# Performance work log

Measured on AMD Instinct MI355X. Metric: run time of the kernel, lower is better.

Reference implementation:

```python
import itertools
import jax, jax.numpy as jnp
import numpy as np

LATENT_DIM = 8
N = 2 * LATENT_DIM  # width of z_combined = concat([z, dz])
BATCH = 131072

# Static combinatorial index sets, matching the nested-loop order
# (i <= j [<= k]) of the torch implementation exactly.
_PAIRS = np.array(list(itertools.combinations_with_replacement(range(N), 2)), dtype=np.int32)   # [136, 2]
_TRIPLES = np.array(list(itertools.combinations_with_replacement(range(N), 3)), dtype=np.int32)  # [816, 3]


def setup_inputs() -> dict:
    key = jax.random.key(0)
    k1, k2 = jax.random.split(key)
    z = jax.random.normal(k1, (BATCH, LATENT_DIM), dtype=jnp.float32)
    dz = jax.random.normal(k2, (BATCH, LATENT_DIM), dtype=jnp.float32)
    return {"z": z, "dz": dz}


def reference(z, dz):
    # z, dz: [B, latent_dim] -> Theta: [B, 985]
    zc = jnp.concatenate([z, dz], axis=1)  # [B, N]
    B = zc.shape[0]
    ones = jnp.ones((B, 1), dtype=zc.dtype)
    # degree-2 terms: zc[:, i] * zc[:, j] for i <= j, all at once via gather
    deg2 = zc[:, _PAIRS[:, 0]] * zc[:, _PAIRS[:, 1]]  # [B, 136]
    # degree-3 terms: zc[:, i] * zc[:, j] * zc[:, k] for i <= j <= k
    deg3 = zc[:, _TRIPLES[:, 0]] * zc[:, _TRIPLES[:, 1]] * zc[:, _TRIPLES[:, 2]]  # [B, 816]
    sine = jnp.sin(zc)  # [B, N]
    return jnp.concatenate([ones, zc, deg2, deg3, sine], axis=1)  # [B, 985]
```

## Files before the change

kernel.cpp:

```cpp
#include <hip/hip_runtime.h>
#include <cstddef>

#define NCOLS 985
#define TROWS 4
#define TILEF (TROWS * NCOLS)
#define NT4   (TILEF / 4)
#define GSTR  176

__global__ __launch_bounds__(256) void sindy_kernel(const float* __restrict__ z,
                                                    const float* __restrict__ dz,
                                                    float* __restrict__ out, int batch,
                                                    int ntiles) {
  __shared__ unsigned short mtab[1024];
  __shared__ unsigned short ptab[136];
  __shared__ float G[4][GSTR];
  __shared__ alignas(16) float rowbuf[TILEF];

  const int tid = threadIdx.x;

  for (int e = tid; e < 1024; e += 256) {
    int a, b;
    if (e < 153)       { a = (e == 0) ? 0 : e; b = 0; }
    else if (e < 969)  {
      int t = e - 153, i = 0;
      for (;;) { int c = (16 - i) * (17 - i) / 2; if (t < c) break; t -= c; ++i; }
      int j = i; while (t >= 16 - j) { t -= 16 - j; ++j; }
      int k = j + t;
      int p = i * 16 - i * (i - 1) / 2 + (j - i);
      a = 17 + p; b = 1 + k;
    }
    else if (e < 985)  { a = 153 + (e - 969); b = 0; }
    else               { a = 169; b = 169; }
    mtab[e] = (unsigned short)(a | (b << 8));
  }
  for (int e = tid; e < 136; e += 256) {
    int p = e, i = 0; while (p >= 16 - i) { p -= 16 - i; ++i; }
    ptab[e] = (unsigned short)(i | ((i + p) << 4));
  }
  __syncthreads();

  const int w = tid >> 6, l = tid & 63;

  unsigned short mt[16];
  #pragma unroll
  for (int wd = 0; wd < 16; ++wd) mt[wd] = mtab[wd * 64 + l];
  const unsigned pe0 = ptab[l];
  const unsigned pe1 = ptab[64 + l];
  const unsigned pe2 = ptab[(128 + l < 136) ? (128 + l) : 135];

  float* Gw = G[w];

  for (int tile = blockIdx.x; tile < ntiles; tile += gridDim.x) {
    const int trow0 = tile * TROWS;
    const int row   = trow0 + w;
    const int nrows = (batch - trow0 < TROWS) ? (batch - trow0) : TROWS;

    if (row < batch) {
      float gval = 0.f;
      if (l == 0)       gval = 1.0f;
      else if (l < 9)   gval = z [(size_t)row * 8 + (l - 1)];
      else if (l < 17)  gval = dz[(size_t)row * 8 + (l - 9)];
      const int gaddr = (l < 17) ? l : (152 + l);
      if (l < 24) Gw[gaddr] = gval;

      const float sv = __shfl(gval, l + 1);
      if (l < 16) Gw[153 + l] = __sinf(sv);
      __builtin_amdgcn_sched_barrier(0);

      {
        float a0 = Gw[1 + (pe0 & 15)], b0 = Gw[1 + (pe0 >> 4)];
        Gw[17 + l] = a0 * b0;
        float a1 = Gw[1 + (pe1 & 15)], b1 = Gw[1 + (pe1 >> 4)];
        Gw[17 + 64 + l] = a1 * b1;
        if (l < 8) {
          float a2 = Gw[1 + (pe2 & 15)], b2 = Gw[1 + (pe2 >> 4)];
          Gw[17 + 128 + l] = a2 * b2;
        }
      }
      __builtin_amdgcn_sched_barrier(0);

      float* rb = rowbuf + w * NCOLS;
      #pragma unroll
      for (int wd = 0; wd < 16; ++wd) {
        const unsigned e = mt[wd];
        const float v = Gw[e & 255] * Gw[e >> 8];
        if (wd < 15)              rb[wd * 64 + l] = v;
        else if (l < NCOLS - 960) rb[960 + l] = v;
      }
    }
    __syncthreads();

    if (nrows == TROWS) {
      float4* __restrict__ dst = (float4*)(out + (size_t)tile * TILEF);
      const float4* srcq = (const float4*)rowbuf;
      #pragma unroll 4
      for (int u = tid; u < NT4; u += 256) {
        dst[u] = srcq[u];
      }
    } else {
      const int nel = nrows * NCOLS;
      float* __restrict__ dst = out + (size_t)tile * TILEF;
      for (int u = tid; u < nel; u += 256) dst[u] = rowbuf[u];
    }
    __syncthreads();
  }
}

extern "C" void kernel_launch(void* const* d_in, const int* in_sizes, int n_in,
                              void* d_out, int out_size, void* d_ws, size_t ws_size,
                              hipStream_t stream) {
  const float* z  = (const float*)d_in[0];
  const float* dz = (const float*)d_in[1];
  float* out = (float*)d_out;
  const int batch = in_sizes[0] / 8;

  const int ntiles = (batch + TROWS - 1) / TROWS;
  const int blocks = 1792;
  sindy_kernel<<<blocks, 256, 0, stream>>>(z, dz, out, batch, ntiles);
}
```

Baseline: 120.9 us.

## Double-buffer row tiles so compute of the next tile overlaps global stores

Adds a second shared-memory tile buffer so each block stores the previous tile to global memory while computing the next one. This drops one __syncthreads per tile. It also rewrites the cubic-term lookup table to use 16-bit offsets into G, and raises the grid from 1792 to 2048 blocks. Shared memory per block roughly doubles, which may lower occupancy. The store-bound kernel may gain little from the overlap.

Result: faster. 117.2 us (-3.1%).

```diff
diff --git a/kernel.cpp b/kernel.cpp
--- a/kernel.cpp
+++ b/kernel.cpp
@@ -4,34 +4,32 @@
 #define NCOLS 985
 #define TROWS 4
 #define TILEF (TROWS * NCOLS)
-#define NT4   (TILEF / 4)
+#define NU    (TILEF / 4)
 #define GSTR  176
 
 __global__ __launch_bounds__(256) void sindy_kernel(const float* __restrict__ z,
                                                     const float* __restrict__ dz,
                                                     float* __restrict__ out, int batch,
                                                     int ntiles) {
-  __shared__ unsigned short mtab[1024];
+  __shared__ unsigned int ctab[1024];
   __shared__ unsigned short ptab[136];
-  __shared__ float G[4][GSTR];
-  __shared__ alignas(16) float rowbuf[TILEF];
+  __shared__ float G4[4][GSTR];
+  __shared__ alignas(16) float buf[2][TILEF];
 
   const int tid = threadIdx.x;
 
-  for (int e = tid; e < 1024; e += 256) {
-    int a, b;
-    if (e < 153)       { a = (e == 0) ? 0 : e; b = 0; }
-    else if (e < 969)  {
-      int t = e - 153, i = 0;
-      for (;;) { int c = (16 - i) * (17 - i) / 2; if (t < c) break; t -= c; ++i; }
-      int j = i; while (t >= 16 - j) { t -= 16 - j; ++j; }
-      int k = j + t;
-      int p = i * 16 - i * (i - 1) / 2 + (j - i);
-      a = 17 + p; b = 1 + k;
+  for (int c = tid; c < 1024; c += 256) {
+    unsigned goff, midx;
+    if (c < 153)      { goff = (unsigned)c; midx = 0; }
+    else if (c < 969) {
+      int t = c - 153, i = 0;
+      for (;;) { int cnt = (16 - i) * (17 - i) / 2; if (t < cnt) break; t -= cnt; ++i; }
+      goff = (unsigned)(17 + (136 - (16 - i) * (17 - i) / 2) + t);
+      midx = (unsigned)(1 + i);
     }
-    else if (e < 985)  { a = 153 + (e - 969); b = 0; }
-    else               { a = 169; b = 169; }
-    mtab[e] = (unsigned short)(a | (b << 8));
+    else if (c < 985) { goff = (unsigned)(153 + (c - 969)); midx = 0; }
+    else              { goff = 169; midx = 169; }
+    ctab[c] = goff | (midx << 16);
   }
   for (int e = tid; e < 136; e += 256) {
     int p = e, i = 0; while (p >= 16 - i) { p -= 16 - i; ++i; }
@@ -41,68 +39,84 @@
 
   const int w = tid >> 6, l = tid & 63;
 
-  unsigned short mt[16];
+  unsigned ct[16];
   #pragma unroll
-  for (int wd = 0; wd < 16; ++wd) mt[wd] = mtab[wd * 64 + l];
+  for (int s = 0; s < 16; ++s) ct[s] = ctab[s * 64 + l];
   const unsigned pe0 = ptab[l];
   const unsigned pe1 = ptab[64 + l];
   const unsigned pe2 = ptab[(128 + l < 136) ? (128 + l) : 135];
 
-  float* Gw = G[w];
+  float* Gw = G4[w];
 
-  for (int tile = blockIdx.x; tile < ntiles; tile += gridDim.x) {
-    const int trow0 = tile * TROWS;
-    const int row   = trow0 + w;
-    const int nrows = (batch - trow0 < TROWS) ? (batch - trow0) : TROWS;
+  auto compute_row = [&](int row, float* rb) {
+    float gval = 0.f;
+    if (l == 0)       gval = 1.0f;
+    else if (l < 9)   gval = z [(size_t)row * 8 + (l - 1)];
+    else if (l < 17)  gval = dz[(size_t)row * 8 + (l - 9)];
+    const int gaddr = (l < 17) ? l : (152 + l);
+    if (l < 24) Gw[gaddr] = gval;
 
-    if (row < batch) {
-      float gval = 0.f;
-      if (l == 0)       gval = 1.0f;
-      else if (l < 9)   gval = z [(size_t)row * 8 + (l - 1)];
-      else if (l < 17)  gval = dz[(size_t)row * 8 + (l - 9)];
-      const int gaddr = (l < 17) ? l : (152 + l);
-      if (l < 24) Gw[gaddr] = gval;
+    const float sv = __shfl(gval, l + 1);
+    if (l < 16) Gw[153 + l] = __sinf(sv);
+    __builtin_amdgcn_sched_barrier(0);
 
-      const float sv = __shfl(gval, l + 1);
-      if (l < 16) Gw[153 + l] = __sinf(sv);
-      __builtin_amdgcn_sched_barrier(0);
-
-      {
-        float a0 = Gw[1 + (pe0 & 15)], b0 = Gw[1 + (pe0 >> 4)];
-        Gw[17 + l] = a0 * b0;
-        float a1 = Gw[1 + (pe1 & 15)], b1 = Gw[1 + (pe1 >> 4)];
-        Gw[17 + 64 + l] = a1 * b1;
-        if (l < 8) {
-          float a2 = Gw[1 + (pe2 & 15)], b2 = Gw[1 + (pe2 >> 4)];
-          Gw[17 + 128 + l] = a2 * b2;
-        }
-      }
-      __builtin_amdgcn_sched_barrier(0);
-
-      float* rb = rowbuf + w * NCOLS;
-      #pragma unroll
-      for (int wd = 0; wd < 16; ++wd) {
-        const unsigned e = mt[wd];
-        const float v = Gw[e & 255] * Gw[e >> 8];
-        if (wd < 15)              rb[wd * 64 + l] = v;
-        else if (l < NCOLS - 960) rb[960 + l] = v;
+    {
+      float a0 = Gw[1 + (pe0 & 15)], b0 = Gw[1 + (pe0 >> 4)];
+      Gw[17 + l] = a0 * b0;
+      float a1 = Gw[1 + (pe1 & 15)], b1 = Gw[1 + (pe1 >> 4)];
+      Gw[17 + 64 + l] = a1 * b1;
+      if (l < 8) {
+        float a2 = Gw[1 + (pe2 & 15)], b2 = Gw[1 + (pe2 >> 4)];
+        Gw[17 + 128 + l] = a2 * b2;
       }
     }
-    __syncthreads();
+    __builtin_amdgcn_sched_barrier(0);
 
-    if (nrows == TROWS) {
-      float4* __restrict__ dst = (float4*)(out + (size_t)tile * TILEF);
-      const float4* srcq = (const float4*)rowbuf;
-      #pragma unroll 4
-      for (int u = tid; u < NT4; u += 256) {
-        dst[u] = srcq[u];
+    #pragma unroll
+    for (int s = 0; s < 16; ++s) {
+      const unsigned e = ct[s];
+      const float v = Gw[e & 0xffffu] * Gw[e >> 16];
+      if (s < 15)      rb[s * 64 + l] = v;
+      else if (l < 25) rb[960 + l] = v;
+    }
+  };
+
+  auto drain_tile = [&](const float* src, float4* __restrict__ dst, int nelem) {
+    if (nelem == TILEF) {
+      const float4* s4 = (const float4*)src;
+      #pragma unroll
+      for (int k = 0; k < 4; ++k) {
+        const int u = k * 256 + tid;
+        if (k < 3 || u < NU) dst[u] = s4[u];
       }
     } else {
-      const int nel = nrows * NCOLS;
-      float* __restrict__ dst = out + (size_t)tile * TILEF;
-      for (int u = tid; u < nel; u += 256) dst[u] = rowbuf[u];
+      float* __restrict__ d = (float*)dst;
+      for (int u = tid; u < nelem; u += 256) d[u] = src[u];
+    }
+  };
+
+  int t = blockIdx.x;
+  if (t >= ntiles) return;
+  int p = 0;
+  {
+    const int row = t * TROWS + w;
+    if (row < batch) compute_row(row, buf[0] + w * NCOLS);
+  }
+  __syncthreads();
+
+  for (int tn = t + gridDim.x; tn < ntiles; tn += gridDim.x) {
+    const int nel = min(TILEF, batch * NCOLS - t * TILEF);
+    drain_tile(buf[p], (float4*)(out + (size_t)t * TILEF), nel);
+    {
+      const int row = tn * TROWS + w;
+      if (row < batch) compute_row(row, buf[p ^ 1] + w * NCOLS);
     }
     __syncthreads();
+    p ^= 1; t = tn;
+  }
+  {
+    const int nel = min(TILEF, batch * NCOLS - t * TILEF);
+    drain_tile(buf[p], (float4*)(out + (size_t)t * TILEF), nel);
   }
 }
 
@@ -115,6 +129,6 @@
   const int batch = in_sizes[0] / 8;
 
   const int ntiles = (batch + TROWS - 1) / TROWS;
-  const int blocks = 1792;
+  const int blocks = 2048;
   sindy_kernel<<<blocks, 256, 0, stream>>>(z, dz, out, batch, ntiles);
 }
```
